# Kernel optimization log

Hardware: AMD Instinct MI355X
Metric: run time of the kernel (lower is better)

The kernel has to match this reference:

```python
import jax, jax.numpy as jnp
import numpy as np

EPS = 1e-5

def binarize(x):
    # sign(x) forward, hardtanh straight-through backward (standard BNN STE)
    xc = jnp.clip(x, -1.0, 1.0)
    s = jnp.where(x >= 0, 1.0, -1.0).astype(x.dtype)
    return xc + jax.lax.stop_gradient(s - xc)

def conv3x3(x, w):
    return jax.lax.conv_general_dilated(
        x, w, window_strides=(1, 1), padding=((1, 1), (1, 1)),
        dimension_numbers=('NCHW', 'OIHW', 'NCHW'))

def maxpool2(x):
    return jax.lax.reduce_window(x, -jnp.inf, jax.lax.max,
                                 (1, 1, 2, 2), (1, 1, 2, 2), 'VALID')

def bn(x, g, b):
    # BatchNorm with batch statistics (training mode, biased variance)
    if x.ndim == 4:
        axes, shp = (0, 2, 3), (1, -1, 1, 1)
    else:
        axes, shp = (0,), (1, -1)
    m = jnp.mean(x, axis=axes, keepdims=True)
    v = jnp.var(x, axis=axes, keepdims=True)
    return (x - m) / jnp.sqrt(v + EPS) * g.reshape(shp) + b.reshape(shp)

def setup_inputs() -> dict:
    key = jax.random.key(0)
    ks = jax.random.split(key, 16)
    def n(i, shape, s=1.0):
        return jax.random.normal(ks[i], shape, dtype=jnp.float32) * s
    B = 256
    inp = {'x': n(0, (B, 3, 32, 32))}
    chans = [(3, 128), (128, 128), (128, 256), (256, 256), (256, 512), (512, 512)]
    for i, (ci, co) in enumerate(chans):
        inp[f'w{i+1}'] = n(1 + i, (co, ci, 3, 3), 0.1)
        inp[f'g{i+1}'] = jnp.ones((co,), jnp.float32)
        inp[f'b{i+1}'] = jnp.zeros((co,), jnp.float32)
    inp['wf1'] = n(7, (1024, 8192), 0.05)
    inp['gf1'] = jnp.ones((1024,), jnp.float32)
    inp['bf1'] = jnp.zeros((1024,), jnp.float32)
    inp['wf2'] = n(8, (10, 1024), 0.05)
    inp['bias2'] = jnp.zeros((10,), jnp.float32)
    inp['gf2'] = jnp.ones((10,), jnp.float32)
    inp['bf2'] = jnp.zeros((10,), jnp.float32)
    return inp

def reference(x, w1, g1, b1, w2, g2, b2, w3, g3, b3, w4, g4, b4,
              w5, g5, b5, w6, g6, b6, wf1, gf1, bf1, wf2, bias2, gf2, bf2):
    # conv1: 3-channel input is NOT binarized (BNN convention)
    h = bn(conv3x3(x, binarize(w1)), g1, b1)
    h = bn(maxpool2(conv3x3(binarize(h), binarize(w2))), g2, b2)
    h = bn(conv3x3(binarize(h), binarize(w3)), g3, b3)
    h = bn(maxpool2(conv3x3(binarize(h), binarize(w4))), g4, b4)
    h = bn(conv3x3(binarize(h), binarize(w5)), g5, b5)
    h = bn(maxpool2(conv3x3(binarize(h), binarize(w6))), g6, b6)
    h = h.reshape(h.shape[0], -1)  # [B, 4*4*512] = [B, 8192]
    h = bn(binarize(h) @ binarize(wf1).T, gf1, bf1)
    h = bn(binarize(h) @ binarize(wf2).T + bias2, gf2, bf2)
    return h
```

## Files before the change

kernel.cpp:

```cpp
#include <hip/hip_runtime.h>
#include <hip/hip_bf16.h>
#include <stdint.h>

static constexpr int BATCH = 256;

#define CDIV(a,b) (((a)+(b)-1)/(b))

__device__ __forceinline__ int BMAC(uint32_t a, uint32_t b, int acc){
  return (int)__popc(a^b) + acc;
}

__global__ void k_pack_conv_w(const float* __restrict__ w, uint32_t* __restrict__ out, int Co, int CW){
  int idx = blockIdx.x*256 + threadIdx.x;
  int total = Co*CW*9;
  if (idx >= total) return;
  int tap = idx % 9; int t = idx / 9; int cw = t % CW; int co = t / CW;
  int Ci = CW*32;
  const float* src = w + ((size_t)co*Ci + (size_t)cw*32)*9 + tap;
  uint32_t bits = 0;
  #pragma unroll
  for (int b=0;b<32;b++) bits |= (src[(size_t)b*9] >= 0.f ? 1u:0u) << b;
  out[idx] = bits;
}

__global__ void k_pack_fc1_w(const float* __restrict__ w, uint32_t* __restrict__ out){
  int idx = blockIdx.x*256 + threadIdx.x;
  if (idx >= 1024*256) return;
  int wd = idx & 255, o = idx >> 8;
  int cw = wd >> 4, p = wd & 15;
  const float* src = w + (size_t)o*8192;
  uint32_t bits=0;
  #pragma unroll
  for (int b=0;b<32;b++) bits |= (src[(cw*32+b)*16 + p] >= 0.f ? 1u:0u) << b;
  out[idx]=bits;
}

__global__ void k_pack_fc2_w(const float* __restrict__ w, uint32_t* __restrict__ out){
  int idx = blockIdx.x*256+threadIdx.x; if (idx >= 10*32) return;
  int wd = idx & 31, o = idx >> 5;
  uint32_t bits=0;
  #pragma unroll
  for (int b=0;b<32;b++) bits |= (w[o*1024 + wd*32 + b] >= 0.f ? 1u:0u)<<b;
  out[idx]=bits;
}

__global__ __launch_bounds__(256) void k_conv1_stats3(const float* __restrict__ x,
        const float* __restrict__ w1, double* __restrict__ partials){
  __shared__ double xs[3][10][34];
  __shared__ float wf[128][27];
  int n = blockIdx.x >> 2, rg = blockIdx.x & 3;
  int y0 = rg*8;
  const float* xp = x + (size_t)n*3*1024;
  for (int i=threadIdx.x; i<3*10*34; i+=256){
    int ci = i/340, r = i%340, ly = r/34, lx = r%34;
    int gy = y0 - 1 + ly, gx = lx - 1;
    double v = 0.0;
    if (gy>=0 && gy<32 && gx>=0 && gx<32) v = (double)xp[ci*1024 + gy*32 + gx];
    (&xs[0][0][0])[i] = v;
  }
  for (int i=threadIdx.x; i<128*27; i+=256)
    (&wf[0][0])[i] = w1[i];
  __syncthreads();
  int wave = threadIdx.x>>6, lane = threadIdx.x&63;
  int c0 = (wave&1)*64, rsub = wave>>1;
  int co = c0 + lane;
  double w[27];
  #pragma unroll
  for (int k=0;k<27;k++) w[k] = (wf[co][k] >= 0.f) ? 1.0 : -1.0;
  double s=0.0, s2=0.0;
  for (int rr = rsub*4; rr < rsub*4+4; ++rr){
    for (int xx=0; xx<32; ++xx){
      double a0=0.0, a1=0.0, a2=0.0;
      #pragma unroll
      for (int ci=0;ci<3;ci++){
        const double* r0 = &xs[ci][rr+0][xx];
        const double* r1 = &xs[ci][rr+1][xx];
        const double* r2 = &xs[ci][rr+2][xx];
        a0 += r0[0]*w[ci*9+0] + r0[1]*w[ci*9+1] + r0[2]*w[ci*9+2];
        a1 += r1[0]*w[ci*9+3] + r1[1]*w[ci*9+4] + r1[2]*w[ci*9+5];
        a2 += r2[0]*w[ci*9+6] + r2[1]*w[ci*9+7] + r2[2]*w[ci*9+8];
      }
      double acc = (a0 + a1) + a2;
      s += acc; s2 += acc*acc;
    }
  }
  size_t pi = (size_t)co*2048 + (size_t)n*8 + rg*2 + rsub;
  partials[pi*2+0]=s; partials[pi*2+1]=s2;
}

__global__ __launch_bounds__(256) void k_finalize_partials_p(const double* __restrict__ partials,
        const float* __restrict__ g, const float* __restrict__ b,
        double* __restrict__ A, double* __restrict__ Bv, int nPart, double invCount){
  int c = blockIdx.x;
  double s=0.0, s2=0.0;
  for (int i=threadIdx.x; i<nPart; i+=256){
    s  += partials[((size_t)c*nPart+i)*2+0];
    s2 += partials[((size_t)c*nPart+i)*2+1];
  }
  for (int off=32; off; off>>=1){ s+=__shfl_down(s,off,64); s2+=__shfl_down(s2,off,64); }
  __shared__ double sh[8];
  int wid=threadIdx.x>>6, lane=threadIdx.x&63;
  if(lane==0){sh[wid]=s;sh[4+wid]=s2;}
  __syncthreads();
  if(threadIdx.x==0){
    double S=0,S2=0;
    #pragma unroll
    for(int i=0;i<4;i++){S+=sh[i];S2+=sh[4+i];}
    double m=S*invCount, v=S2*invCount-m*m;
    double a=(double)g[c]/sqrt(v+1e-5);
    A[c]=a; Bv[c]=(double)b[c]-m*a;
  }
}

__global__ __launch_bounds__(256) void k_conv1_binarize5(const float* __restrict__ x,
        const float* __restrict__ w1, const double* __restrict__ A, const double* __restrict__ Bv,
        uint32_t* __restrict__ bits){
  __shared__ double xs[3][6][34];
  __shared__ float wf[128][27];
  __shared__ uint32_t wordbuf[4][128];
  int n = blockIdx.x >> 3, rg = blockIdx.x & 7;
  int y0 = rg*4;
  const float* xp = x + (size_t)n*3*1024;
  for (int i=threadIdx.x; i<3*6*34; i+=256){
    int ci = i/204, r = i%204, ly = r/34, lx = r%34;
    int gy = y0 - 1 + ly, gx = lx - 1;
    double v = 0.0;
    if (gy>=0 && gy<32 && gx>=0 && gx<32) v = (double)xp[ci*1024 + gy*32 + gx];
    (&xs[0][0][0])[i] = v;
  }
  for (int i=threadIdx.x; i<128*27; i+=256)
    (&wf[0][0])[i] = w1[i];
  __syncthreads();
  int wave = threadIdx.x>>6, lane = threadIdx.x&63;
  int c0 = (wave&1)*64, rsub = wave>>1;
  int co = c0 + lane;
  double w[27];
  #pragma unroll
  for (int k=0;k<27;k++) w[k] = (wf[co][k] >= 0.f) ? 1.0 : -1.0;
  double av = A[co], bv = Bv[co];
  for (int rr = rsub*2; rr < rsub*2+2; ++rr){
    for (int x0=0; x0<32; x0+=4){
      double acc[4] = {0,0,0,0};
      #pragma unroll
      for (int ci=0;ci<3;ci++)
        #pragma unroll
        for (int ky=0;ky<3;ky++){
          const double* r = &xs[ci][rr+ky][x0];
          double v0=r[0],v1=r[1],v2=r[2],v3=r[3],v4=r[4],v5=r[5];
          double w0=w[ci*9+ky*3+0], w1v=w[ci*9+ky*3+1], w2=w[ci*9+ky*3+2];
          acc[0] += v0*w0 + v1*w1v + v2*w2;
          acc[1] += v1*w0 + v2*w1v + v3*w2;
          acc[2] += v2*w0 + v3*w1v + v4*w2;
          acc[3] += v3*w0 + v4*w1v + v5*w2;
        }
      #pragma unroll
      for (int j=0;j<4;j++){
        int pred = (acc[j]*av + bv >= 0.0) ? 1 : 0;
        unsigned long long m = __ballot(pred);
        if (lane == 0){
          int p = rr*32 + x0 + j;
          wordbuf[(c0>>5)+0][p] = (uint32_t)m;
          wordbuf[(c0>>5)+1][p] = (uint32_t)(m>>32);
        }
      }
    }
  }
  __syncthreads();
  for (int i=threadIdx.x; i<512; i+=256){
    int cw = i>>7, p = i&127;
    bits[(size_t)n*4096 + cw*1024 + rg*128 + p] = wordbuf[cw][p];
  }
}

template<int CW,int H,int W,int HP,int PITCH>
__device__ __forceinline__ void stage_bits(const uint32_t* __restrict__ ip, uint32_t* __restrict__ inlds){
  for (int i=threadIdx.x; i<CW*HP*PITCH; i+=256) inlds[i]=0u;
}

template<int CW,int H,int W,int HP,int PITCH>
__device__ __forceinline__ void fill_bits(const uint32_t* __restrict__ ip, uint32_t* __restrict__ inlds){
  constexpr int LOGW  = (W==32)?5:(W==16)?4:3;
  constexpr int LOGHW = ((H*W)==1024)?10:((H*W)==256)?8:6;
  for (int i=threadIdx.x; i<CW*H*W; i+=256){
    int cw = i >> LOGHW;
    int rem = i & (H*W-1);
    int y = rem >> LOGW;
    int x = rem & (W-1);
    inlds[cw*HP*PITCH + (y+1)*PITCH + (x+1)] = ip[i];
  }
}

template<int CW,int H,int W,int CO,int COB,int NX>
__global__ __launch_bounds__(256) void k_xconv_pool2(const uint32_t* __restrict__ in,
        const uint32_t* __restrict__ wb, int16_t* __restrict__ out, long long* __restrict__ part){
  constexpr int HP = H+2;
  constexpr int PITCH = W+3;
  constexpr int WP = CW*9+1;
  constexpr int NG = CO/COB;
  constexpr int XS = W/NX;
  constexpr int UNITS = (H/2)*XS;
  static_assert((COB/2)*UNITS==256, "thread mapping");
  __shared__ uint32_t inlds[CW*HP*PITCH];
  __shared__ uint32_t wlds[COB*WP];
  __shared__ int colpc[COB][10];
  int n = blockIdx.x / NG, cg = blockIdx.x % NG;
  int co0 = cg*COB;
  const uint32_t* ip = in + (size_t)n*CW*H*W;
  stage_bits<CW,H,W,HP,PITCH>(ip, inlds);
  for (int i=threadIdx.x; i<COB*CW*9; i+=256){
    int co = i/(CW*9); int r = i%(CW*9);
    wlds[co*WP + r] = wb[(size_t)(co0+co)*CW*9 + r];
  }
  __syncthreads();
  fill_bits<CW,H,W,HP,PITCH>(ip, inlds);
  for (int i=threadIdx.x; i<COB*9; i+=256){
    int co=i/9, tap=i%9; int s=0;
    #pragma unroll
    for (int cw=0;cw<CW;cw++) s += __popc(wlds[co*WP + cw*9 + tap]);
    colpc[co][tap]=s;
  }
  __syncthreads();
  int t = threadIdx.x;
  int cog = t / UNITS;
  int rem = t % UNITS;
  int yy = rem / XS;
  int xs = (rem % XS)*NX;
  int c0 = cog*2;
  int acc0[2][NX], acc1[2][NX];
  #pragma unroll
  for (int c=0;c<2;c++)
    #pragma unroll
    for (int i2=0;i2<NX;i2++){acc0[c][i2]=0;acc1[c][i2]=0;}
  for (int cw=0; cw<CW; cw++){
    uint32_t wr[2][9];
    #pragma unroll
    for (int c=0;c<2;c++)
      #pragma unroll
      for (int k=0;k<9;k++) wr[c][k]=wlds[(c0+c)*WP+cw*9+k];
    const uint32_t* ib = &inlds[cw*HP*PITCH + (2*yy)*PITCH + xs];
    {
      uint32_t row[NX+2];
      #pragma unroll
      for (int j=0;j<NX+2;j++) row[j] = ib[j];
      #pragma unroll
      for (int q=0;q<NX;q++)
        #pragma unroll
        for (int c=0;c<2;c++){
          acc0[c][q] = BMAC(row[q],  wr[c][0], acc0[c][q]);
          acc0[c][q] = BMAC(row[q+1],wr[c][1], acc0[c][q]);
          acc0[c][q] = BMAC(row[q+2],wr[c][2], acc0[c][q]);
        }
    }
    #pragma unroll
    for (int rrow=1; rrow<=2; rrow++){
      uint32_t row[NX+2];
      #pragma unroll
      for (int j=0;j<NX+2;j++) row[j] = ib[rrow*PITCH + j];
      #pragma unroll
      for (int q=0;q<NX;q++)
        #pragma unroll
        for (int c=0;c<2;c++){
          acc0[c][q] = BMAC(row[q],  wr[c][3*rrow+0], acc0[c][q]);
          acc0[c][q] = BMAC(row[q+1],wr[c][3*rrow+1], acc0[c][q]);
          acc0[c][q] = BMAC(row[q+2],wr[c][3*rrow+2], acc0[c][q]);
          acc1[c][q] = BMAC(row[q],  wr[c][3*rrow-3], acc1[c][q]);
          acc1[c][q] = BMAC(row[q+1],wr[c][3*rrow-2], acc1[c][q]);
          acc1[c][q] = BMAC(row[q+2],wr[c][3*rrow-1], acc1[c][q]);
        }
    }
    {
      uint32_t row[NX+2];
      #pragma unroll
      for (int j=0;j<NX+2;j++) row[j] = ib[3*PITCH + j];
      #pragma unroll
      for (int q=0;q<NX;q++)
        #pragma unroll
        for (int c=0;c<2;c++){
          acc1[c][q] = BMAC(row[q],  wr[c][6], acc1[c][q]);
          acc1[c][q] = BMAC(row[q+1],wr[c][7], acc1[c][q]);
          acc1[c][q] = BMAC(row[q+2],wr[c][8], acc1[c][q]);
        }
    }
  }
  #pragma unroll
  for (int c=0;c<2;c++){
    const int* cp = colpc[c0+c];
    int16_t res[NX/2];
    #pragma unroll
    for (int tp=0; tp<NX/2; tp++){
      int best=-32768;
      #pragma unroll
      for (int rrow=0;rrow<2;rrow++){
        int kyi = (rrow==0 && yy==0) ? 0 : ((rrow==1 && yy==H/2-1) ? 2 : -1);
        #pragma unroll
        for (int dx=0;dx<2;dx++){
          int q = 2*tp+dx;
          int x = xs+q;
          int kxi = (x==0)?0:((x==W-1)?2:-1);
          int acc = rrow? acc1[c][q]:acc0[c][q];
          int corr=0, nv=9;
          if (kyi>=0){ corr += cp[kyi*3+0]+cp[kyi*3+1]+cp[kyi*3+2]; }
          if (kxi>=0){ corr += cp[0+kxi]+cp[3+kxi]+cp[6+kxi]; }
          if (kyi>=0 && kxi>=0){ corr -= cp[kyi*3+kxi]; nv=4; }
          else if (kyi>=0 || kxi>=0) nv=6;
          int dot = 32*CW*nv - 2*(acc - corr);
          best = dot>best?dot:best;
        }
      }
      res[tp]=(int16_t)best;
    }
    int16_t* op = out + (((size_t)n*CO + (co0+c0+c))*(H/2) + yy)*(W/2) + xs/2;
    #pragma unroll
    for (int tp=0;tp<NX/2;tp++) op[tp]=res[tp];
    int ssum=0; long long ssq=0;
    #pragma unroll
    for (int tp=0;tp<NX/2;tp++){ int v=res[tp]; ssum+=v; ssq += (long long)(v*v); }
    long long s = (long long)ssum;
    #pragma unroll
    for (int off=UNITS>>1; off; off>>=1){ s += __shfl_down(s,off,UNITS); ssq += __shfl_down(ssq,off,UNITS); }
    if (rem==0){
      size_t pi = (size_t)(co0+c0+c)*BATCH + n;
      part[pi*2+0]=s; part[pi*2+1]=ssq;
    }
  }
}

template<int CW,int H,int W,int CO,int COB,int NX>
__global__ __launch_bounds__(256) void k_xconv_pool(const uint32_t* __restrict__ in,
        const uint32_t* __restrict__ wb, int16_t* __restrict__ out, long long* __restrict__ part){
  constexpr int HP = H+2;
  constexpr int PITCH = W+3;
  constexpr int WP = CW*9+1;
  constexpr int NG = CO/COB;
  constexpr int XS = W/NX;
  constexpr int UNITS = (H/2)*XS;
  static_assert(COB*UNITS==256, "thread mapping");
  __shared__ uint32_t inlds[CW*HP*PITCH];
  __shared__ uint32_t wlds[COB*WP];
  __shared__ int colpc[COB][10];
  int n = blockIdx.x / NG, cg = blockIdx.x % NG;
  int co0 = cg*COB;
  const uint32_t* ip = in + (size_t)n*CW*H*W;
  stage_bits<CW,H,W,HP,PITCH>(ip, inlds);
  for (int i=threadIdx.x; i<COB*CW*9; i+=256){
    int co = i/(CW*9); int r = i%(CW*9);
    wlds[co*WP + r] = wb[(size_t)(co0+co)*CW*9 + r];
  }
  __syncthreads();
  fill_bits<CW,H,W,HP,PITCH>(ip, inlds);
  for (int i=threadIdx.x; i<COB*9; i+=256){
    int co=i/9, tap=i%9; int s=0;
    #pragma unroll
    for (int cw=0;cw<CW;cw++) s += __popc(wlds[co*WP + cw*9 + tap]);
    colpc[co][tap]=s;
  }
  __syncthreads();
  int t = threadIdx.x;
  int col = t / UNITS;
  int rem = t % UNITS;
  int yy = rem / XS;
  int xs = (rem % XS)*NX;
  int co = co0 + col;
  int acc0[NX], acc1[NX];
  #pragma unroll
  for (int i2=0;i2<NX;i2++){acc0[i2]=0;acc1[i2]=0;}
  for (int cw=0; cw<CW; cw++){
    uint32_t wr[9];
    #pragma unroll
    for (int k=0;k<9;k++) wr[k]=wlds[col*WP+cw*9+k];
    const uint32_t* ib = &inlds[cw*HP*PITCH + (2*yy)*PITCH + xs];
    {
      uint32_t row[NX+2];
      #pragma unroll
      for (int j=0;j<NX+2;j++) row[j] = ib[j];
      #pragma unroll
      for (int q=0;q<NX;q++){
        acc0[q] = BMAC(row[q],  wr[0], acc0[q]);
        acc0[q] = BMAC(row[q+1],wr[1], acc0[q]);
        acc0[q] = BMAC(row[q+2],wr[2], acc0[q]);
      }
    }
    #pragma unroll
    for (int rrow=1; rrow<=2; rrow++){
      uint32_t row[NX+2];
      #pragma unroll
      for (int j=0;j<NX+2;j++) row[j] = ib[rrow*PITCH + j];
      #pragma unroll
      for (int q=0;q<NX;q++){
        acc0[q] = BMAC(row[q],  wr[3*rrow+0], acc0[q]);
        acc0[q] = BMAC(row[q+1],wr[3*rrow+1], acc0[q]);
        acc0[q] = BMAC(row[q+2],wr[3*rrow+2], acc0[q]);
        acc1[q] = BMAC(row[q],  wr[3*rrow-3], acc1[q]);
        acc1[q] = BMAC(row[q+1],wr[3*rrow-2], acc1[q]);
        acc1[q] = BMAC(row[q+2],wr[3*rrow-1], acc1[q]);
      }
    }
    {
      uint32_t row[NX+2];
      #pragma unroll
      for (int j=0;j<NX+2;j++) row[j] = ib[3*PITCH + j];
      #pragma unroll
      for (int q=0;q<NX;q++){
        acc1[q] = BMAC(row[q],  wr[6], acc1[q]);
        acc1[q] = BMAC(row[q+1],wr[7], acc1[q]);
        acc1[q] = BMAC(row[q+2],wr[8], acc1[q]);
      }
    }
  }
  const int* cp = colpc[col];
  int16_t res[NX/2];
  #pragma unroll
  for (int tp=0; tp<NX/2; tp++){
    int best=-32768;
    #pragma unroll
    for (int rrow=0;rrow<2;rrow++){
      int kyi = (rrow==0 && yy==0) ? 0 : ((rrow==1 && yy==H/2-1) ? 2 : -1);
      #pragma unroll
      for (int dx=0;dx<2;dx++){
        int q = 2*tp+dx;
        int x = xs+q;
        int kxi = (x==0)?0:((x==W-1)?2:-1);
        int acc = rrow? acc1[q]:acc0[q];
        int corr=0, nv=9;
        if (kyi>=0){ corr += cp[kyi*3+0]+cp[kyi*3+1]+cp[kyi*3+2]; }
        if (kxi>=0){ corr += cp[0+kxi]+cp[3+kxi]+cp[6+kxi]; }
        if (kyi>=0 && kxi>=0){ corr -= cp[kyi*3+kxi]; nv=4; }
        else if (kyi>=0 || kxi>=0) nv=6;
        int dot = 32*CW*nv - 2*(acc - corr);
        best = dot>best?dot:best;
      }
    }
    res[tp]=(int16_t)best;
  }
  int16_t* op = out + (((size_t)n*CO + co)*(H/2) + yy)*(W/2) + xs/2;
  #pragma unroll
  for (int tp=0;tp<NX/2;tp++) op[tp]=res[tp];
  int ssum=0; long long ssq=0;
  #pragma unroll
  for (int tp=0;tp<NX/2;tp++){ int v=res[tp]; ssum+=v; ssq += (long long)(v*v); }
  long long s = (long long)ssum;
  #pragma unroll
  for (int off=UNITS>>1; off; off>>=1){ s += __shfl_down(s,off,UNITS); ssq += __shfl_down(ssq,off,UNITS); }
  if (rem==0){
    size_t pi = (size_t)co*BATCH + n;
    part[pi*2+0]=s; part[pi*2+1]=ssq;
  }
}

template<int CW,int H,int W,int CO,int COB,int NX>
__global__ __launch_bounds__(256) void k_xconv(const uint32_t* __restrict__ in,
        const uint32_t* __restrict__ wb, int16_t* __restrict__ out, long long* __restrict__ part){
  constexpr int HP = H+2;
  constexpr int PITCH = W+3;
  constexpr int WP = CW*9+1;
  constexpr int NG = CO/COB;
  constexpr int XS = W/NX;
  constexpr int UNITS = H*XS;
  static_assert((COB/2)*UNITS==256, "thread mapping");
  __shared__ uint32_t inlds[CW*HP*PITCH];
  __shared__ uint32_t wlds[COB*WP];
  __shared__ int colpc[COB][10];
  int n = blockIdx.x / NG, cg = blockIdx.x % NG;
  int co0 = cg*COB;
  const uint32_t* ip = in + (size_t)n*CW*H*W;
  stage_bits<CW,H,W,HP,PITCH>(ip, inlds);
  for (int i=threadIdx.x; i<COB*CW*9; i+=256){
    int co = i/(CW*9); int r = i%(CW*9);
    wlds[co*WP + r] = wb[(size_t)(co0+co)*CW*9 + r];
  }
  __syncthreads();
  fill_bits<CW,H,W,HP,PITCH>(ip, inlds);
  for (int i=threadIdx.x; i<COB*9; i+=256){
    int co=i/9, tap=i%9; int s=0;
    #pragma unroll
    for (int cw=0;cw<CW;cw++) s += __popc(wlds[co*WP + cw*9 + tap]);
    colpc[co][tap]=s;
  }
  __syncthreads();
  int t = threadIdx.x;
  int cog = t / UNITS;
  int rem = t % UNITS;
  int y = rem / XS;
  int xs = (rem % XS)*NX;
  int c0 = cog*2;
  int acc[2][NX];
  #pragma unroll
  for (int c=0;c<2;c++)
    #pragma unroll
    for (int i2=0;i2<NX;i2++) acc[c][i2]=0;
  for (int cw=0; cw<CW; cw++){
    uint32_t wr[2][9];
    #pragma unroll
    for (int c=0;c<2;c++)
      #pragma unroll
      for (int k=0;k<9;k++) wr[c][k]=wlds[(c0+c)*WP+cw*9+k];
    const uint32_t* ib = &inlds[cw*HP*PITCH + y*PITCH + xs];
    #pragma unroll
    for (int rrow=0; rrow<3; rrow++){
      uint32_t row[NX+2];
      #pragma unroll
      for (int j=0;j<NX+2;j++) row[j] = ib[rrow*PITCH + j];
      #pragma unroll
      for (int q=0;q<NX;q++){
        acc[0][q] = BMAC(row[q],  wr[0][3*rrow+0], acc[0][q]);
        acc[0][q] = BMAC(row[q+1],wr[0][3*rrow+1], acc[0][q]);
        acc[0][q] = BMAC(row[q+2],wr[0][3*rrow+2], acc[0][q]);
        acc[1][q] = BMAC(row[q],  wr[1][3*rrow+0], acc[1][q]);
        acc[1][q] = BMAC(row[q+1],wr[1][3*rrow+1], acc[1][q]);
        acc[1][q] = BMAC(row[q+2],wr[1][3*rrow+2], acc[1][q]);
      }
    }
  }
  int kyi = (y==0)?0:((y==H-1)?2:-1);
  #pragma unroll
  for (int c=0;c<2;c++){
    const int* cp = colpc[c0+c];
    int16_t rbuf[NX];
    int ssum=0; long long ssq=0;
    #pragma unroll
    for (int q=0;q<NX;q++){
      int x = xs+q;
      int kxi = (x==0)?0:((x==W-1)?2:-1);
      int corr=0, nv=9;
      if (kyi>=0){ corr += cp[kyi*3+0]+cp[kyi*3+1]+cp[kyi*3+2]; }
      if (kxi>=0){ corr += cp[0+kxi]+cp[3+kxi]+cp[6+kxi]; }
      if (kyi>=0 && kxi>=0){ corr -= cp[kyi*3+kxi]; nv=4; }
      else if (kyi>=0 || kxi>=0) nv=6;
      int dot = 32*CW*nv - 2*(acc[c][q] - corr);
      rbuf[q] = (int16_t)dot;
      ssum+=dot; ssq+=(long long)(dot*dot);
    }
    int16_t* op = out + (((size_t)n*CO + (co0+c0+c))*H + y)*W + xs;
    #pragma unroll
    for (int q=0;q<NX;q++) op[q]=rbuf[q];
    long long s=(long long)ssum, q2=ssq;
    #pragma unroll
    for (int off=UNITS>>1; off; off>>=1){ s += __shfl_down(s,off,UNITS); q2 += __shfl_down(q2,off,UNITS); }
    if (rem==0){
      size_t pi = (size_t)(co0+c0+c)*BATCH + n;
      part[pi*2+0]=s; part[pi*2+1]=q2;
    }
  }
}

__global__ __launch_bounds__(256) void k_chstats_fin_p(const long long* __restrict__ part,
        const float* __restrict__ g, const float* __restrict__ b,
        double* __restrict__ A, double* __restrict__ Bv, double invCount){
  int c = blockIdx.x;
  long long s  = part[((size_t)c*BATCH+threadIdx.x)*2+0];
  long long s2 = part[((size_t)c*BATCH+threadIdx.x)*2+1];
  for (int off=32; off; off>>=1){ s+=__shfl_down(s,off,64); s2+=__shfl_down(s2,off,64); }
  __shared__ long long sh[8];
  int wid=threadIdx.x>>6, lane=threadIdx.x&63;
  if(lane==0){sh[wid]=s;sh[4+wid]=s2;}
  __syncthreads();
  if(threadIdx.x==0){
    long long S=0,S2=0;
    #pragma unroll
    for(int i=0;i<4;i++){S+=sh[i];S2+=sh[4+i];}
    double m=(double)S*invCount, v=(double)S2*invCount-m*m;
    double a=(double)g[c]/sqrt(v+1e-5);
    A[c]=a; Bv[c]=(double)b[c]-m*a;
  }
}

__global__ void k_binarize_pack(const int16_t* __restrict__ in, const double* __restrict__ A,
                                const double* __restrict__ Bv, uint32_t* __restrict__ bits,
                                int C, int HW){
  int CW = C>>5;
  size_t total = (size_t)BATCH*CW*HW;
  size_t idx = (size_t)blockIdx.x*256+threadIdx.x;
  if (idx>=total) return;
  int hw = (int)(idx % HW); size_t t = idx/HW;
  int cw = (int)(t % CW); int n = (int)(t / CW);
  uint32_t wordv=0;
  for (int b=0;b<32;b++){
    int c = cw*32+b;
    double v = (double)in[((size_t)n*C + c)*HW + hw];
    if (v*A[c]+Bv[c] >= 0.0) wordv |= 1u<<b;
  }
  bits[idx]=wordv;
}

__global__ void k_fc1(const uint32_t* __restrict__ actbits, const uint32_t* __restrict__ wb,
                      int16_t* __restrict__ out){
  int og = blockIdx.x & 3; int n = blockIdx.x >> 2;
  int o = og*256 + threadIdx.x;
  __shared__ uint32_t sact[256];
  sact[threadIdx.x] = actbits[(size_t)n*256 + threadIdx.x];
  __syncthreads();
  const uint32_t* wp = wb + (size_t)o*256;
  int acc=0;
  #pragma unroll 8
  for (int k=0;k<256;k++) acc = BMAC(sact[k], wp[k], acc);
  out[(size_t)n*1024 + o] = (int16_t)(8192 - 2*acc);
}

__global__ void k_fc_stats(const int16_t* __restrict__ in, const float* __restrict__ g,
                           const float* __restrict__ b, double* __restrict__ A, double* __restrict__ Bv){
  int f = blockIdx.x;
  double v = (double)in[(size_t)threadIdx.x*1024 + f];
  double s=v, s2=v*v;
  __shared__ double sh[8];
  for (int off=32; off; off>>=1){ s+=__shfl_down(s,off,64); s2+=__shfl_down(s2,off,64); }
  int wid=threadIdx.x>>6, lane=threadIdx.x&63;
  if(lane==0){sh[wid]=s;sh[4+wid]=s2;}
  __syncthreads();
  if(threadIdx.x==0){
    double S=0,S2=0;
    #pragma unroll
    for(int i=0;i<4;i++){S+=sh[i];S2+=sh[4+i];}
    double m=S/256.0, var=S2/256.0-m*m;
    double a=(double)g[f]/sqrt(var+1e-5);
    A[f]=a; Bv[f]=(double)b[f]-m*a;
  }
}

__global__ void k_binpack_fc(const int16_t* __restrict__ in, const double* __restrict__ A,
                             const double* __restrict__ Bv, uint32_t* __restrict__ bits){
  int idx = blockIdx.x*256+threadIdx.x;
  if (idx >= 256*32) return;
  int w = idx & 31, n = idx >> 5;
  uint32_t word=0;
  for (int b=0;b<32;b++){
    int f = w*32+b;
    double v=(double)in[(size_t)n*1024+f];
    if (v*A[f]+Bv[f] >= 0.0) word|=1u<<b;
  }
  bits[idx]=word;
}

__global__ void k_fc2_out(const uint32_t* __restrict__ actbits, const uint32_t* __restrict__ wb,
                          const float* __restrict__ bias2, const float* __restrict__ g,
                          const float* __restrict__ b, float* __restrict__ out){
  int o = blockIdx.x;
  int n = threadIdx.x;
  const uint32_t* ap = actbits + (size_t)n*32;
  const uint32_t* wp = wb + (size_t)o*32;
  int acc=0;
  #pragma unroll
  for (int k=0;k<32;k++) acc = BMAC(ap[k], wp[k], acc);
  double h = (double)(1024 - 2*acc) + (double)bias2[o];
  double s=h, s2=h*h;
  __shared__ double sh[8];
  for(int off=32;off;off>>=1){s+=__shfl_down(s,off,64);s2+=__shfl_down(s2,off,64);}
  int wid=threadIdx.x>>6,lane=threadIdx.x&63;
  if(lane==0){sh[wid]=s;sh[4+wid]=s2;}
  __syncthreads();
  __shared__ double sm, sinv;
  if(threadIdx.x==0){
    double S=0,S2=0;
    #pragma unroll
    for(int i=0;i<4;i++){S+=sh[i];S2+=sh[4+i];}
    double m=S/256.0, v=S2/256.0-m*m;
    sm=m; sinv=1.0/sqrt(v+1e-5);
  }
  __syncthreads();
  double r = (h - sm)*sinv*(double)g[o] + (double)b[o];
  out[(size_t)n*10 + o] = (float)r;
}

extern "C" void kernel_launch(void* const* d_in, const int* in_sizes, int n_in,
                              void* d_out, int out_size, void* d_ws, size_t ws_size,
                              hipStream_t stream) {
  const float* x   = (const float*)d_in[0];
  const float* w1  = (const float*)d_in[1];
  const float* g1  = (const float*)d_in[2];
  const float* b1  = (const float*)d_in[3];
  const float* w2  = (const float*)d_in[4];
  const float* g2  = (const float*)d_in[5];
  const float* b2  = (const float*)d_in[6];
  const float* w3  = (const float*)d_in[7];
  const float* g3  = (const float*)d_in[8];
  const float* b3  = (const float*)d_in[9];
  const float* w4  = (const float*)d_in[10];
  const float* g4  = (const float*)d_in[11];
  const float* b4  = (const float*)d_in[12];
  const float* w5  = (const float*)d_in[13];
  const float* g5  = (const float*)d_in[14];
  const float* b5  = (const float*)d_in[15];
  const float* w6  = (const float*)d_in[16];
  const float* g6  = (const float*)d_in[17];
  const float* b6  = (const float*)d_in[18];
  const float* wf1 = (const float*)d_in[19];
  const float* gf1 = (const float*)d_in[20];
  const float* bf1 = (const float*)d_in[21];
  const float* wf2 = (const float*)d_in[22];
  const float* bias2=(const float*)d_in[23];
  const float* gf2 = (const float*)d_in[24];
  const float* bf2 = (const float*)d_in[25];
  float* out = (float*)d_out;

  char* ws = (char*)d_ws;
  size_t off = 0;
  auto alloc = [&](size_t bytes)->char*{ char* p = ws + off; off = (off + bytes + 255) & ~(size_t)255; return p; };

  uint32_t* wb2  = (uint32_t*)alloc(4608ull*4);
  uint32_t* wb3  = (uint32_t*)alloc(9216ull*4);
  uint32_t* wb4  = (uint32_t*)alloc(18432ull*4);
  uint32_t* wb5  = (uint32_t*)alloc(36864ull*4);
  uint32_t* wb6  = (uint32_t*)alloc(73728ull*4);
  uint32_t* wf1b = (uint32_t*)alloc(262144ull*4);
  uint32_t* wf2b = (uint32_t*)alloc(320ull*4);
  double*   part = (double*)  alloc(128ull*2048*2*8);
  long long* pll = (long long*)alloc(512ull*256*2*8);
  double*   Abuf = (double*)  alloc(1024ull*8);
  double*   Bbuf = (double*)  alloc(1024ull*8);
  uint32_t* bitsA= (uint32_t*)alloc(1048576ull*4);
  uint32_t* bitsB= (uint32_t*)alloc(262144ull*4);
  int16_t*  conv = (int16_t*) alloc(16777216ull*2);

  k_pack_conv_w<<<CDIV(4608,256),256,0,stream>>>(w2, wb2, 128, 4);
  k_pack_conv_w<<<CDIV(9216,256),256,0,stream>>>(w3, wb3, 256, 4);
  k_pack_conv_w<<<CDIV(18432,256),256,0,stream>>>(w4, wb4, 256, 8);
  k_pack_conv_w<<<CDIV(36864,256),256,0,stream>>>(w5, wb5, 512, 8);
  k_pack_conv_w<<<CDIV(73728,256),256,0,stream>>>(w6, wb6, 512, 16);
  k_pack_fc1_w<<<CDIV(262144,256),256,0,stream>>>(wf1, wf1b);
  k_pack_fc2_w<<<CDIV(320,256),256,0,stream>>>(wf2, wf2b);

  k_conv1_stats3<<<1024,256,0,stream>>>(x, w1, part);
  k_finalize_partials_p<<<128,256,0,stream>>>(part, g1, b1, Abuf, Bbuf, 2048, 1.0/(256.0*1024.0));
  k_conv1_binarize5<<<2048,256,0,stream>>>(x, w1, Abuf, Bbuf, bitsA);

  k_xconv_pool2<4,32,32,128,8,8><<<256*16,256,0,stream>>>(bitsA, wb2, conv, pll);
  k_chstats_fin_p<<<128,256,0,stream>>>(pll, g2, b2, Abuf, Bbuf, 1.0/(256.0*256.0));
  k_binarize_pack<<<CDIV(256ull*4*256,256),256,0,stream>>>(conv, Abuf, Bbuf, bitsB, 128, 256);

  k_xconv<4,16,16,256,16,8><<<256*16,256,0,stream>>>(bitsB, wb3, conv, pll);
  k_chstats_fin_p<<<256,256,0,stream>>>(pll, g3, b3, Abuf, Bbuf, 1.0/(256.0*256.0));
  k_binarize_pack<<<CDIV(256ull*8*256,256),256,0,stream>>>(conv, Abuf, Bbuf, bitsA, 256, 256);

  k_xconv_pool2<8,16,16,256,32,8><<<256*8,256,0,stream>>>(bitsA, wb4, conv, pll);
  k_chstats_fin_p<<<256,256,0,stream>>>(pll, g4, b4, Abuf, Bbuf, 1.0/(256.0*64.0));
  k_binarize_pack<<<CDIV(256ull*8*64,256),256,0,stream>>>(conv, Abuf, Bbuf, bitsB, 256, 64);

  k_xconv<8,8,8,512,64,8><<<256*8,256,0,stream>>>(bitsB, wb5, conv, pll);
  k_chstats_fin_p<<<512,256,0,stream>>>(pll, g5, b5, Abuf, Bbuf, 1.0/(256.0*64.0));
  k_binarize_pack<<<CDIV(256ull*16*64,256),256,0,stream>>>(conv, Abuf, Bbuf, bitsA, 512, 64);

  k_xconv_pool<16,8,8,512,64,8><<<256*8,256,0,stream>>>(bitsA, wb6, conv, pll);
  k_chstats_fin_p<<<512,256,0,stream>>>(pll, g6, b6, Abuf, Bbuf, 1.0/(256.0*16.0));
  k_binarize_pack<<<CDIV(256ull*16*16,256),256,0,stream>>>(conv, Abuf, Bbuf, bitsB, 512, 16);

  k_fc1<<<256*4,256,0,stream>>>(bitsB, wf1b, conv);
  k_fc_stats<<<1024,256,0,stream>>>(conv, gf1, bf1, Abuf, Bbuf);
  k_binpack_fc<<<CDIV(256*32,256),256,0,stream>>>(conv, Abuf, Bbuf, bitsA);

  k_fc2_out<<<10,256,0,stream>>>(bitsA, wf2b, bias2, gf2, bf2, out);

  (void)in_sizes; (void)n_in; (void)out_size; (void)ws_size;
}
```

Baseline: 634.6 us.

## Register-block conv1 stats over 4 pixels, split rows finer, merge weight packing

The conv1 statistics kernel now computes four adjacent output pixels per inner iteration and reuses six loaded shared-memory values across them, instead of reloading each 3-tap window per pixel. It also launches twice as many blocks, each covering 4 rows instead of 8, so the partials buffer and the finalize count double to 4096 per channel. The five per-layer conv weight-packing launches are merged into one kernel that picks the layer by index range, cutting launch overhead. The cost is more register pressure from the fp64 accumulators and a larger partials reduction.

Measured after the change: 618.1 us. 1.03x faster.

```diff
diff --git a/kernel.cpp b/kernel.cpp
--- a/kernel.cpp
+++ b/kernel.cpp
@@ -10,17 +10,25 @@
   return (int)__popc(a^b) + acc;
 }
 
-__global__ void k_pack_conv_w(const float* __restrict__ w, uint32_t* __restrict__ out, int Co, int CW){
+__global__ void k_pack_conv_all(const float* __restrict__ w2,const float* __restrict__ w3,
+        const float* __restrict__ w4,const float* __restrict__ w5,const float* __restrict__ w6,
+        uint32_t* __restrict__ o2,uint32_t* __restrict__ o3,uint32_t* __restrict__ o4,
+        uint32_t* __restrict__ o5,uint32_t* __restrict__ o6){
   int idx = blockIdx.x*256 + threadIdx.x;
-  int total = Co*CW*9;
-  if (idx >= total) return;
-  int tap = idx % 9; int t = idx / 9; int cw = t % CW; int co = t / CW;
+  const float* w; uint32_t* o; int CW; int rel;
+  if      (idx <   4608){ w=w2; o=o2; CW=4;  rel=idx; }
+  else if (idx <  13824){ w=w3; o=o3; CW=4;  rel=idx-4608; }
+  else if (idx <  32256){ w=w4; o=o4; CW=8;  rel=idx-13824; }
+  else if (idx <  69120){ w=w5; o=o5; CW=8;  rel=idx-32256; }
+  else if (idx < 142848){ w=w6; o=o6; CW=16; rel=idx-69120; }
+  else return;
+  int tap = rel % 9; int t = rel / 9; int cw = t % CW; int co = t / CW;
   int Ci = CW*32;
   const float* src = w + ((size_t)co*Ci + (size_t)cw*32)*9 + tap;
   uint32_t bits = 0;
   #pragma unroll
   for (int b=0;b<32;b++) bits |= (src[(size_t)b*9] >= 0.f ? 1u:0u) << b;
-  out[idx] = bits;
+  o[rel] = bits;
 }
 
 __global__ void k_pack_fc1_w(const float* __restrict__ w, uint32_t* __restrict__ out){
@@ -44,15 +52,15 @@
   out[idx]=bits;
 }
 
-__global__ __launch_bounds__(256) void k_conv1_stats3(const float* __restrict__ x,
+__global__ __launch_bounds__(256) void k_conv1_stats4(const float* __restrict__ x,
         const float* __restrict__ w1, double* __restrict__ partials){
-  __shared__ double xs[3][10][34];
+  __shared__ double xs[3][6][34];
   __shared__ float wf[128][27];
-  int n = blockIdx.x >> 2, rg = blockIdx.x & 3;
-  int y0 = rg*8;
+  int n = blockIdx.x >> 3, rg = blockIdx.x & 7;
+  int y0 = rg*4;
   const float* xp = x + (size_t)n*3*1024;
-  for (int i=threadIdx.x; i<3*10*34; i+=256){
-    int ci = i/340, r = i%340, ly = r/34, lx = r%34;
+  for (int i=threadIdx.x; i<3*6*34; i+=256){
+    int ci = i/204, r = i%204, ly = r/34, lx = r%34;
     int gy = y0 - 1 + ly, gx = lx - 1;
     double v = 0.0;
     if (gy>=0 && gy<32 && gx>=0 && gx<32) v = (double)xp[ci*1024 + gy*32 + gx];
@@ -68,23 +76,26 @@
   #pragma unroll
   for (int k=0;k<27;k++) w[k] = (wf[co][k] >= 0.f) ? 1.0 : -1.0;
   double s=0.0, s2=0.0;
-  for (int rr = rsub*4; rr < rsub*4+4; ++rr){
-    for (int xx=0; xx<32; ++xx){
-      double a0=0.0, a1=0.0, a2=0.0;
-      #pragma unroll
-      for (int ci=0;ci<3;ci++){
-        const double* r0 = &xs[ci][rr+0][xx];
-        const double* r1 = &xs[ci][rr+1][xx];
-        const double* r2 = &xs[ci][rr+2][xx];
-        a0 += r0[0]*w[ci*9+0] + r0[1]*w[ci*9+1] + r0[2]*w[ci*9+2];
-        a1 += r1[0]*w[ci*9+3] + r1[1]*w[ci*9+4] + r1[2]*w[ci*9+5];
-        a2 += r2[0]*w[ci*9+6] + r2[1]*w[ci*9+7] + r2[2]*w[ci*9+8];
-      }
-      double acc = (a0 + a1) + a2;
-      s += acc; s2 += acc*acc;
-    }
-  }
-  size_t pi = (size_t)co*2048 + (size_t)n*8 + rg*2 + rsub;
+  for (int rr = rsub*2; rr < rsub*2+2; ++rr){
+    for (int x0=0; x0<32; x0+=4){
+      double acc[4] = {0,0,0,0};
+      #pragma unroll
+      for (int ci=0;ci<3;ci++)
+        #pragma unroll
+        for (int ky=0;ky<3;ky++){
+          const double* r = &xs[ci][rr+ky][x0];
+          double v0=r[0],v1=r[1],v2=r[2],v3=r[3],v4=r[4],v5=r[5];
+          double w0=w[ci*9+ky*3+0], w1v=w[ci*9+ky*3+1], w2=w[ci*9+ky*3+2];
+          acc[0] += v0*w0 + v1*w1v + v2*w2;
+          acc[1] += v1*w0 + v2*w1v + v3*w2;
+          acc[2] += v2*w0 + v3*w1v + v4*w2;
+          acc[3] += v3*w0 + v4*w1v + v5*w2;
+        }
+      #pragma unroll
+      for (int j=0;j<4;j++){ s += acc[j]; s2 += acc[j]*acc[j]; }
+    }
+  }
+  size_t pi = (size_t)co*4096 + (size_t)n*16 + rg*2 + rsub;
   partials[pi*2+0]=s; partials[pi*2+1]=s2;
 }
 
@@ -702,7 +713,7 @@
   uint32_t* wb6  = (uint32_t*)alloc(73728ull*4);
   uint32_t* wf1b = (uint32_t*)alloc(262144ull*4);
   uint32_t* wf2b = (uint32_t*)alloc(320ull*4);
-  double*   part = (double*)  alloc(128ull*2048*2*8);
+  double*   part = (double*)  alloc(128ull*4096*2*8);
   long long* pll = (long long*)alloc(512ull*256*2*8);
   double*   Abuf = (double*)  alloc(1024ull*8);
   double*   Bbuf = (double*)  alloc(1024ull*8);
@@ -710,16 +721,12 @@
   uint32_t* bitsB= (uint32_t*)alloc(262144ull*4);
   int16_t*  conv = (int16_t*) alloc(16777216ull*2);
 
-  k_pack_conv_w<<<CDIV(4608,256),256,0,stream>>>(w2, wb2, 128, 4);
-  k_pack_conv_w<<<CDIV(9216,256),256,0,stream>>>(w3, wb3, 256, 4);
-  k_pack_conv_w<<<CDIV(18432,256),256,0,stream>>>(w4, wb4, 256, 8);
-  k_pack_conv_w<<<CDIV(36864,256),256,0,stream>>>(w5, wb5, 512, 8);
-  k_pack_conv_w<<<CDIV(73728,256),256,0,stream>>>(w6, wb6, 512, 16);
+  k_pack_conv_all<<<CDIV(142848,256),256,0,stream>>>(w2,w3,w4,w5,w6, wb2,wb3,wb4,wb5,wb6);
   k_pack_fc1_w<<<CDIV(262144,256),256,0,stream>>>(wf1, wf1b);
   k_pack_fc2_w<<<CDIV(320,256),256,0,stream>>>(wf2, wf2b);
 
-  k_conv1_stats3<<<1024,256,0,stream>>>(x, w1, part);
-  k_finalize_partials_p<<<128,256,0,stream>>>(part, g1, b1, Abuf, Bbuf, 2048, 1.0/(256.0*1024.0));
+  k_conv1_stats4<<<2048,256,0,stream>>>(x, w1, part);
+  k_finalize_partials_p<<<128,256,0,stream>>>(part, g1, b1, Abuf, Bbuf, 4096, 1.0/(256.0*1024.0));
   k_conv1_binarize5<<<2048,256,0,stream>>>(x, w1, Abuf, Bbuf, bitsA);
 
   k_xconv_pool2<4,32,32,128,8,8><<<256*16,256,0,stream>>>(bitsA, wb2, conv, pll);
```
